# Kernel optimization log

Measured on AMD Instinct MI355X. Metric: run time of the kernel, lower is better.

The kernel has to match this reference:

```python
import jax, jax.numpy as jnp
import numpy as np

B, N, DIM = 4, 2048, 64  # batch, seq_len (== gate out dim), model dim (== dim_head)
H, DH = 8, 64            # heads, dim_head


def setup_inputs() -> dict:
    key = jax.random.key(0)
    ks = jax.random.split(key, 12)
    inner = H * DH
    inp = {
        'q': jax.random.normal(ks[0], (B, N, DIM), jnp.float32),
        'k': jax.random.normal(ks[1], (B, N, DIM), jnp.float32),
        'v': jax.random.normal(ks[2], (B, N, DIM), jnp.float32),
        'Wq': jax.random.normal(ks[3], (inner, DIM), jnp.float32) * 0.05,
        'Wk': jax.random.normal(ks[4], (inner, DIM), jnp.float32) * 0.05,
        'Wv': jax.random.normal(ks[5], (inner, DIM), jnp.float32) * 0.05,
        'Wo': jax.random.normal(ks[6], (DIM, inner), jnp.float32) * 0.05,
        'bo': jax.random.normal(ks[7], (DIM,), jnp.float32) * 0.05,
        'Wg': jax.random.normal(ks[8], (N, DIM), jnp.float32) * 0.05,
        's_local': jnp.float32(1.0),
        's_long': jnp.float32(1.0),
        # recurrent compressive-memory state; positive to avoid 0/0 of zero-init buffers
        'mem': jax.random.uniform(ks[9], (H, DH, DH), jnp.float32) + 0.5,
        'mem_norm': jax.random.uniform(ks[10], (H, N, 1), jnp.float32) + 0.5,
    }
    return inp


def _heads(x, W):
    # x: (B,N,DIM) @ W.T (DIM, H*DH) -> (B,H,N,DH)
    y = x @ W.T
    return y.reshape(x.shape[0], x.shape[1], H, DH).transpose(0, 2, 1, 3)


def reference(q, k, v, Wq, Wk, Wv, Wo, bo, Wg, s_local, s_long, mem, mem_norm):
    scale = DH ** -0.5
    qh, kh, vh = _heads(q, Wq), _heads(k, Wk), _heads(v, Wv)  # (B,H,N,DH)

    # local softmax attention, down-gated by (1 - sigmoid(local scalar))
    sim = jnp.einsum('bhnd,bhmd->bhnm', qh, kh) * scale
    local_attn = jax.nn.softmax(sim, axis=-1) * (1.0 - jax.nn.sigmoid(s_local))

    # query compressive memory: elu(q) @ M / (elu(q) * norm)
    eq = jax.nn.elu(qh)
    mem_q = jnp.einsum('bhnd,hde->bhne', eq, mem) / (eq * mem_norm[None])  # (B,H,N,DH)
    gated = jax.nn.sigmoid(s_long) * jnp.einsum('bhnd,md->bhnm', mem_q, Wg)  # (B,H,N,N)

    attn = local_attn + gated
    out = jnp.einsum('bhnm,bhmd->bhnd', attn, vh)
    out = out.transpose(0, 2, 1, 3).reshape(q.shape[0], q.shape[1], H * DH)
    out = out @ Wo.T + bo  # (B,N,DIM)

    # memory update (state side effect in the original forward)
    ek = jax.nn.elu(kh)
    v_term = vh - jnp.einsum('bhnd,hde->bhne', ek, mem) / (ek * mem_norm[None])
    new_mem = mem[None] + jnp.einsum('bhnd,bhne->bhde', ek, v_term)  # (B,H,DH,DH)
    new_norm = ek.sum(-1)  # (B,H,N)
    return out, new_mem, new_norm
```

## Files before the change

kernel.cpp:

```cpp
#include <hip/hip_runtime.h>
#include <math.h>


#define B_   4
#define N_   2048
#define H_   8
#define BH_  32
#define KP   72
#define KPV  68
#define SCLK 0.18033688f

typedef __bf16 bf16x8 __attribute__((ext_vector_type(8)));
typedef __bf16 bf16x4 __attribute__((ext_vector_type(4)));
typedef short  s16x4  __attribute__((ext_vector_type(4)));
typedef float  f32x4  __attribute__((ext_vector_type(4)));

__device__ __forceinline__ float eluf(float x) {
    return x > 0.0f ? x : expm1f(x);
}

__device__ __forceinline__ float fexp2(float x) {
    return __builtin_amdgcn_exp2f(x);
}

__device__ __forceinline__ f32x4 mfma16(bf16x4 a, bf16x4 b, f32x4 c) {
#if __has_builtin(__builtin_amdgcn_mfma_f32_16x16x16_bf16)
    return __builtin_amdgcn_mfma_f32_16x16x16_bf16(a, b, c, 0, 0, 0);
#else
    s16x4 ai, bi;
    __builtin_memcpy(&ai, &a, 8);
    __builtin_memcpy(&bi, &b, 8);
    return __builtin_amdgcn_mfma_f32_16x16x16bf16_1k(ai, bi, c, 0, 0, 0);
#endif
}

__global__ __launch_bounds__(256) void k_proj(
    const float* __restrict__ q, const float* __restrict__ k, const float* __restrict__ v,
    const float* __restrict__ Wq, const float* __restrict__ Wk, const float* __restrict__ Wv,
    __bf16* __restrict__ qb, float* __restrict__ kh, __bf16* __restrict__ kb,
    __bf16* __restrict__ vb, __bf16* __restrict__ vbT)
{
    const int which = blockIdx.z;
    const int h    = blockIdx.y;
    const int row0 = blockIdx.x * 64;
    const int tid  = threadIdx.x;
    const int b = row0 >> 11, nb = row0 & 2047;

    __shared__ __align__(16) float  AsT[64][68];
    __shared__ __align__(16) float  WsT[64][68];
    __shared__ __align__(16) __bf16 Cs[64 * 72];

    if (which == 2) {
        const int w = tid >> 6, lane = tid & 63;
        const int quad = lane >> 4, m = lane & 15;
        const float* ar = v + (size_t)(row0 + w * 16 + m) * 64;
        bf16x8 a0, a1;
        #pragma unroll
        for (int j = 0; j < 8; ++j) {
            a0[j] = (__bf16)ar[quad * 8 + j];
            a1[j] = (__bf16)ar[32 + quad * 8 + j];
        }
        f32x4 acc[4];
        #pragma unroll
        for (int t = 0; t < 4; ++t) {
            const float* wr = Wv + (size_t)(h * 64 + t * 16 + m) * 64;
            bf16x8 b0, b1;
            #pragma unroll
            for (int j = 0; j < 8; ++j) {
                b0[j] = (__bf16)wr[quad * 8 + j];
                b1[j] = (__bf16)wr[32 + quad * 8 + j];
            }
            f32x4 z = {0.f, 0.f, 0.f, 0.f};
            z = __builtin_amdgcn_mfma_f32_16x16x32_bf16(a0, b0, z, 0, 0, 0);
            acc[t] = __builtin_amdgcn_mfma_f32_16x16x32_bf16(a1, b1, z, 0, 0, 0);
        }
        #pragma unroll
        for (int t = 0; t < 4; ++t)
            #pragma unroll
            for (int r = 0; r < 4; ++r)
                Cs[(w * 16 + quad * 4 + r) * 72 + t * 16 + m] = (__bf16)acc[t][r];
        __syncthreads();
        const int rr = tid >> 2, csg = (tid & 3) * 16;
        bf16x8 r0 = *(const bf16x8*)&Cs[rr * 72 + csg];
        bf16x8 r1 = *(const bf16x8*)&Cs[rr * 72 + csg + 8];
        size_t gb = ((((size_t)b * H_ + h) * N_ + nb + rr) << 6) + csg;
        *(bf16x8*)&vb[gb]     = r0;
        *(bf16x8*)&vb[gb + 8] = r1;
        const int e = tid >> 2, ns = (tid & 3) * 16;
        bf16x8 t0, t1;
        #pragma unroll
        for (int j = 0; j < 8; ++j) {
            t0[j] = Cs[(ns + j) * 72 + e];
            t1[j] = Cs[(ns + 8 + j) * 72 + e];
        }
        size_t base = (((size_t)b * H_ + h) * 64 + e) * (size_t)N_ + nb + ns;
        *(bf16x8*)&vbT[base]     = t0;
        *(bf16x8*)&vbT[base + 8] = t1;
        return;
    }

    const float* __restrict__ src = (which == 0) ? q : k;
    const float* __restrict__ W   = (which == 0) ? Wq : Wk;
    for (int s = 0; s < 16; ++s) {
        int flat = s * 256 + tid;
        int r = flat >> 6, d = flat & 63;
        AsT[d][r] = src[(size_t)(row0 + r) * 64 + d];
        WsT[d][r] = W[(size_t)(h * 64 + r) * 64 + d];
    }
    __syncthreads();

    const int ty = tid >> 4, tx = tid & 15;
    float acc[4][4];
    #pragma unroll
    for (int i = 0; i < 4; ++i)
        #pragma unroll
        for (int j = 0; j < 4; ++j) acc[i][j] = 0.0f;
    for (int kd = 0; kd < 64; ++kd) {
        float4 a4 = *(const float4*)&AsT[kd][ty * 4];
        float4 w4 = *(const float4*)&WsT[kd][tx * 4];
        float a[4] = {a4.x, a4.y, a4.z, a4.w};
        float w[4] = {w4.x, w4.y, w4.z, w4.w};
        #pragma unroll
        for (int i = 0; i < 4; ++i)
            #pragma unroll
            for (int j = 0; j < 4; ++j) acc[i][j] = fmaf(a[i], w[j], acc[i][j]);
    }

    if (which == 0) {
        #pragma unroll
        for (int i = 0; i < 4; ++i) {
            size_t idx = ((((size_t)b * H_ + h) * N_ + nb + ty * 4 + i) << 6) + tx * 4;
            bf16x4 o4 = {(__bf16)acc[i][0], (__bf16)acc[i][1],
                         (__bf16)acc[i][2], (__bf16)acc[i][3]};
            *(bf16x4*)&qb[idx] = o4;
        }
    } else {
        #pragma unroll
        for (int i = 0; i < 4; ++i) {
            size_t idx = ((((size_t)b * H_ + h) * N_ + nb + ty * 4 + i) << 6) + tx * 4;
            *(float4*)&kh[idx] = make_float4(acc[i][0], acc[i][1], acc[i][2], acc[i][3]);
            bf16x4 o4 = {(__bf16)(acc[i][0] * SCLK), (__bf16)(acc[i][1] * SCLK),
                         (__bf16)(acc[i][2] * SCLK), (__bf16)(acc[i][3] * SCLK)};
            *(bf16x4*)&kb[idx] = o4;
        }
    }
}

__global__ __launch_bounds__(256) void k_memacc(
    const float* __restrict__ kh, const __bf16* __restrict__ vb,
    const float* __restrict__ mem, const float* __restrict__ mem_norm,
    float* __restrict__ pmem, float* __restrict__ out_norm)
{
    const int chunk = blockIdx.x;
    const int bh    = blockIdx.y;
    const int h     = bh & 7;
    const int n0    = chunk * 128;

    __shared__ __align__(16) __bf16 memT_hi[64 * KP], memT_lo[64 * KP];
    __shared__ __align__(16) __bf16 ekn_hi[64 * KP],  ekn_lo[64 * KP];
    __shared__ __align__(16) __bf16 ekT_hi[64 * KP],  ekT_lo[64 * KP];
    __shared__ __align__(16) __bf16 vtT_hi[64 * KP],  vtT_lo[64 * KP];

    const int tid  = threadIdx.x;
    const int w    = tid >> 6, lane = tid & 63;
    const int quad = lane >> 4, m = lane & 15;

    for (int s = 0; s < 16; ++s) {
        int flat = s * 256 + tid;
        int d = flat >> 6, e = flat & 63;
        float mv = mem[(size_t)h * 4096 + flat];
        __bf16 hi = (__bf16)mv;
        memT_hi[e * KP + d] = hi;
        memT_lo[e * KP + d] = (__bf16)(mv - (float)hi);
    }

    bf16x8 onesv;
    #pragma unroll
    for (int j = 0; j < 8; ++j) onesv[j] = (m == 0) ? (__bf16)1.0f : (__bf16)0.0f;

    f32x4 accM[4];
    #pragma unroll
    for (int t = 0; t < 4; ++t) { f32x4 z = {0.f, 0.f, 0.f, 0.f}; accM[t] = z; }
    __syncthreads();

    for (int sub = 0; sub < 2; ++sub) {
        const int nb = n0 + sub * 64;
        for (int rr = w; rr < 64; rr += 4) {
            const int n = nb + rr;
            float ekv = eluf(kh[((size_t)bh * N_ + n) * 64 + lane]);
            __bf16 hi = (__bf16)ekv;
            __bf16 lo = (__bf16)(ekv - (float)hi);
            ekn_hi[rr * KP + lane] = hi;
            ekn_lo[rr * KP + lane] = lo;
            ekT_hi[lane * KP + rr] = hi;
            ekT_lo[lane * KP + rr] = lo;
        }
        __syncthreads();

        f32x4 km[4];
        #pragma unroll
        for (int t = 0; t < 4; ++t) { f32x4 z = {0.f, 0.f, 0.f, 0.f}; km[t] = z; }
        f32x4 nsum = {0.f, 0.f, 0.f, 0.f};
        #pragma unroll
        for (int c2 = 0; c2 < 2; ++c2) {
            bf16x8 Ah = *(const bf16x8*)&ekn_hi[(w * 16 + m) * KP + c2 * 32 + quad * 8];
            bf16x8 Al = *(const bf16x8*)&ekn_lo[(w * 16 + m) * KP + c2 * 32 + quad * 8];
            nsum = __builtin_amdgcn_mfma_f32_16x16x32_bf16(Ah, onesv, nsum, 0, 0, 0);
            nsum = __builtin_amdgcn_mfma_f32_16x16x32_bf16(Al, onesv, nsum, 0, 0, 0);
            #pragma unroll
            for (int et = 0; et < 4; ++et) {
                bf16x8 Bh = *(const bf16x8*)&memT_hi[(et * 16 + m) * KP + c2 * 32 + quad * 8];
                bf16x8 Bl = *(const bf16x8*)&memT_lo[(et * 16 + m) * KP + c2 * 32 + quad * 8];
                km[et] = __builtin_amdgcn_mfma_f32_16x16x32_bf16(Al, Bh, km[et], 0, 0, 0);
                km[et] = __builtin_amdgcn_mfma_f32_16x16x32_bf16(Ah, Bl, km[et], 0, 0, 0);
                km[et] = __builtin_amdgcn_mfma_f32_16x16x32_bf16(Ah, Bh, km[et], 0, 0, 0);
            }
        }
        if (m == 0) {
            #pragma unroll
            for (int r = 0; r < 4; ++r)
                out_norm[(size_t)bh * N_ + nb + w * 16 + quad * 4 + r] = nsum[r];
        }
        float nrmv[4];
        #pragma unroll
        for (int r = 0; r < 4; ++r)
            nrmv[r] = mem_norm[(size_t)h * N_ + nb + w * 16 + quad * 4 + r];
        #pragma unroll
        for (int et = 0; et < 4; ++et) {
            #pragma unroll
            for (int r = 0; r < 4; ++r) {
                const int nl = w * 16 + quad * 4 + r;
                const int e  = et * 16 + m;
                float vh  = (float)vb[((size_t)bh * N_ + nb + nl) * 64 + e];
                float ekv = (float)ekn_hi[nl * KP + e] + (float)ekn_lo[nl * KP + e];
                float vt  = vh - km[et][r] * __builtin_amdgcn_rcpf(ekv * nrmv[r]);
                __bf16 hi = (__bf16)vt;
                vtT_hi[e * KP + nl] = hi;
                vtT_lo[e * KP + nl] = (__bf16)(vt - (float)hi);
            }
        }
        __syncthreads();

        #pragma unroll
        for (int c2 = 0; c2 < 2; ++c2) {
            bf16x8 Ah = *(const bf16x8*)&ekT_hi[(w * 16 + m) * KP + c2 * 32 + quad * 8];
            bf16x8 Al = *(const bf16x8*)&ekT_lo[(w * 16 + m) * KP + c2 * 32 + quad * 8];
            #pragma unroll
            for (int et = 0; et < 4; ++et) {
                bf16x8 Bh = *(const bf16x8*)&vtT_hi[(et * 16 + m) * KP + c2 * 32 + quad * 8];
                bf16x8 Bl = *(const bf16x8*)&vtT_lo[(et * 16 + m) * KP + c2 * 32 + quad * 8];
                accM[et] = __builtin_amdgcn_mfma_f32_16x16x32_bf16(Al, Bh, accM[et], 0, 0, 0);
                accM[et] = __builtin_amdgcn_mfma_f32_16x16x32_bf16(Ah, Bl, accM[et], 0, 0, 0);
                accM[et] = __builtin_amdgcn_mfma_f32_16x16x32_bf16(Ah, Bh, accM[et], 0, 0, 0);
            }
        }
        __syncthreads();
    }

    const size_t base = ((size_t)chunk * BH_ + bh) * 4096;
    #pragma unroll
    for (int et = 0; et < 4; ++et)
        #pragma unroll
        for (int r = 0; r < 4; ++r)
            pmem[base + (size_t)(w * 16 + quad * 4 + r) * 64 + et * 16 + m] =
                accM[et][r];
}

__global__ __launch_bounds__(256) void k_gv(
    const float* __restrict__ Wg, const __bf16* __restrict__ vbT,
    float* __restrict__ pGv)
{
    const int chunk = blockIdx.x;
    const int bh    = blockIdx.y;
    const int n0    = chunk * 128;
    __shared__ __align__(16) __bf16 WgT[64 * 136];
    const int tid  = threadIdx.x;
    const int w    = tid >> 6, lane = tid & 63;
    const int quad = lane >> 4, m = tid & 15;

    for (int s = 0; s < 8; ++s) {
        int f4 = s * 256 + tid;
        int n = f4 >> 4, dg = (f4 & 15) * 4;
        float4 wv = *(const float4*)&Wg[(size_t)(n0 + n) * 64 + dg];
        WgT[(dg + 0) * 136 + n] = (__bf16)wv.x;
        WgT[(dg + 1) * 136 + n] = (__bf16)wv.y;
        WgT[(dg + 2) * 136 + n] = (__bf16)wv.z;
        WgT[(dg + 3) * 136 + n] = (__bf16)wv.w;
    }
    __syncthreads();

    f32x4 acc[4];
    #pragma unroll
    for (int t = 0; t < 4; ++t) { f32x4 z = {0.f, 0.f, 0.f, 0.f}; acc[t] = z; }
    #pragma unroll
    for (int c = 0; c < 4; ++c) {
        bf16x8 Af = *(const bf16x8*)&WgT[(w * 16 + m) * 136 + c * 32 + quad * 8];
        #pragma unroll
        for (int et = 0; et < 4; ++et) {
            bf16x8 Bf = *(const bf16x8*)&vbT[((size_t)bh * 64 + et * 16 + m) * N_ +
                                             n0 + c * 32 + quad * 8];
            acc[et] = __builtin_amdgcn_mfma_f32_16x16x32_bf16(Af, Bf, acc[et], 0, 0, 0);
        }
    }
    const size_t base = ((size_t)chunk * BH_ + bh) * 4096;
    #pragma unroll
    for (int et = 0; et < 4; ++et)
        #pragma unroll
        for (int r = 0; r < 4; ++r)
            pGv[base + (size_t)(w * 16 + quad * 4 + r) * 64 + et * 16 + m] =
                acc[et][r];
}

__global__ __launch_bounds__(256) void k_reduce(
    const float* __restrict__ mem, const float* __restrict__ pmem,
    const float* __restrict__ pGv, float* __restrict__ out_mem, float* __restrict__ Gv)
{
    const int idx = blockIdx.x * 256 + threadIdx.x;
    const int bh = idx >> 12, h = bh & 7, de = idx & 4095;
    float sm = mem[(size_t)h * 4096 + de];
    float sg = 0.0f;
    #pragma unroll
    for (int c = 0; c < 16; ++c) {
        sm += pmem[(size_t)c * 131072 + idx];
        sg += pGv[(size_t)c * 131072 + idx];
    }
    out_mem[idx] = sm;
    Gv[idx] = sg;
}

__global__ __launch_bounds__(512, 2) void k_flash(
    const __bf16* __restrict__ qb, const __bf16* __restrict__ kb,
    const __bf16* __restrict__ vbT, const float* __restrict__ mem,
    const float* __restrict__ mem_norm, const float* __restrict__ Gv,
    const float* __restrict__ s_local_p, const float* __restrict__ s_long_p,
    __bf16* __restrict__ o)
{
    const int n0 = blockIdx.x * 256;
    const int bh = blockIdx.y;
    const int h  = bh & 7;
    const __bf16* __restrict__ kbp = kb  + (size_t)bh * N_ * 64;
    const __bf16* __restrict__ vtp = vbT + (size_t)bh * 64 * N_;

    __shared__ __align__(16) char smem[56832];
    __bf16* const KbA = (__bf16*)(smem);
    __bf16* const KbB = (__bf16*)(smem + 9216);
    __bf16* const VTA = (__bf16*)(smem + 18432);
    __bf16* const VTB = (__bf16*)(smem + 27136);
    __bf16* const MT  = (__bf16*)(smem);
    __bf16* const GT  = (__bf16*)(smem + 9216);
    __bf16* const Pw  = (__bf16*)(smem + 17920);
    float*  const lsl   = (float*)(smem + 54784);
    float*  const nrm_l = (float*)(smem + 55808);

    const int tid  = threadIdx.x;
    const int w    = tid >> 6, lane = tid & 63;
    const int quad = lane >> 4, m = lane & 15;
    const float gl   = 1.0f - 1.0f / (1.0f + __expf(-s_local_p[0]));
    const float sigg = 1.0f / (1.0f + __expf(-s_long_p[0]));

    if (tid < 256) nrm_l[tid] = mem_norm[(size_t)h * N_ + n0 + tid];

    const size_t q0 = ((size_t)bh * N_ + n0 + w * 32 + m) * 64;
    const size_t q1 = q0 + 16 * 64;
    bf16x8 qa00 = *(const bf16x8*)&qb[q0 + quad * 8];
    bf16x8 qa01 = *(const bf16x8*)&qb[q0 + 32 + quad * 8];
    bf16x8 qa10 = *(const bf16x8*)&qb[q1 + quad * 8];
    bf16x8 qa11 = *(const bf16x8*)&qb[q1 + 32 + quad * 8];

    f32x4 O0[4], O1[4];
    #pragma unroll
    for (int t = 0; t < 4; ++t) {
        f32x4 z = {0.f, 0.f, 0.f, 0.f};
        O0[t] = z; O1[t] = z;
    }
    f32x4 nacc0 = {0.f, 0.f, 0.f, 0.f}, nacc1 = {0.f, 0.f, 0.f, 0.f};
    bf16x4 ones4;
    #pragma unroll
    for (int j = 0; j < 4; ++j) ones4[j] = (m == 0) ? (__bf16)1.0f : (__bf16)0.0f;
    const int pr0 = w * 32, pr1 = w * 32 + 16;

    const int srow = tid >> 3, scg = (tid & 7) * 8;
    bf16x8 pk0 = *(const bf16x8*)&kbp[(size_t)srow * 64 + scg];
    bf16x8 pv0 = *(const bf16x8*)&vtp[(size_t)srow * N_ + scg];
    *(bf16x8*)&KbA[srow * KP + scg]  = pk0;
    *(bf16x8*)&VTA[srow * KPV + scg] = pv0;
    {
        const size_t kn = (size_t)(64 + srow) * 64 + scg;
        const size_t vn = (size_t)srow * N_ + 64 + scg;
        pk0 = *(const bf16x8*)&kbp[kn];
        pv0 = *(const bf16x8*)&vtp[vn];
    }

    for (int c = 0; c < 32; ++c) {
        asm volatile("s_waitcnt lgkmcnt(0)" ::: "memory");
        __builtin_amdgcn_s_barrier();
        if (c + 1 < 32) {
            __bf16* Kn = (c & 1) ? KbA : KbB;
            __bf16* Vn = (c & 1) ? VTA : VTB;
            *(bf16x8*)&Kn[srow * KP + scg]  = pk0;
            *(bf16x8*)&Vn[srow * KPV + scg] = pv0;
        }
        if (c + 2 < 32) {
            const size_t kn = (size_t)((c + 2) * 64 + srow) * 64 + scg;
            const size_t vn = (size_t)srow * N_ + (c + 2) * 64 + scg;
            pk0 = *(const bf16x8*)&kbp[kn];
            pv0 = *(const bf16x8*)&vtp[vn];
        }
        const __bf16* Kc = (c & 1) ? KbB : KbA;
        const __bf16* Vc = (c & 1) ? VTB : VTA;

        f32x4 s0[4], s1[4];
        __builtin_amdgcn_s_setprio(1);
        #pragma unroll
        for (int t = 0; t < 4; ++t) {
            bf16x8 ka0 = *(const bf16x8*)&Kc[(t * 16 + m) * KP + quad * 8];
            bf16x8 ka1 = *(const bf16x8*)&Kc[(t * 16 + m) * KP + 32 + quad * 8];
            f32x4 z = {0.f, 0.f, 0.f, 0.f};
            z = __builtin_amdgcn_mfma_f32_16x16x32_bf16(ka0, qa00, z, 0, 0, 0);
            s0[t] = __builtin_amdgcn_mfma_f32_16x16x32_bf16(ka1, qa01, z, 0, 0, 0);
            f32x4 z2 = {0.f, 0.f, 0.f, 0.f};
            z2 = __builtin_amdgcn_mfma_f32_16x16x32_bf16(ka0, qa10, z2, 0, 0, 0);
            s1[t] = __builtin_amdgcn_mfma_f32_16x16x32_bf16(ka1, qa11, z2, 0, 0, 0);
        }
        __builtin_amdgcn_s_setprio(0);

        bf16x4 pa0[4], pa1[4];
        #pragma unroll
        for (int t = 0; t < 4; ++t) {
            float p0 = fexp2(s0[t][0]), p1 = fexp2(s0[t][1]);
            float p2 = fexp2(s0[t][2]), p3 = fexp2(s0[t][3]);
            bf16x4 pk = {(__bf16)p0, (__bf16)p1, (__bf16)p2, (__bf16)p3};
            pa0[t] = pk;
            float r0 = fexp2(s1[t][0]), r1 = fexp2(s1[t][1]);
            float r2 = fexp2(s1[t][2]), r3 = fexp2(s1[t][3]);
            bf16x4 rk = {(__bf16)r0, (__bf16)r1, (__bf16)r2, (__bf16)r3};
            pa1[t] = rk;
        }

        __builtin_amdgcn_s_setprio(1);
        #pragma unroll
        for (int t = 0; t < 4; ++t) {
            nacc0 = mfma16(pa0[t], ones4, nacc0);
            nacc1 = mfma16(pa1[t], ones4, nacc1);
            #pragma unroll
            for (int et = 0; et < 4; ++et) {
                bf16x4 vb4 = *(const bf16x4*)&Vc[(et * 16 + m) * KPV + t * 16 + quad * 4];
                O0[et] = mfma16(pa0[t], vb4, O0[et]);
                O1[et] = mfma16(pa1[t], vb4, O1[et]);
            }
        }
        __builtin_amdgcn_s_setprio(0);
    }

    if (m == 0) {
        #pragma unroll
        for (int r = 0; r < 4; ++r) {
            lsl[pr0 + quad * 4 + r] = nacc0[r];
            lsl[pr1 + quad * 4 + r] = nacc1[r];
        }
    }

    __syncthreads();
    {
        const float* mp = mem + (size_t)h * 4096;
        const float* gp = Gv + (size_t)bh * 4096;
        #pragma unroll
        for (int s2 = 0; s2 < 2; ++s2) {
            int idx = s2 * 512 + tid;
            int e = idx & 63, d4 = (idx >> 6) << 2;
            bf16x4 mv, gv;
            #pragma unroll
            for (int j = 0; j < 4; ++j) {
                mv[j] = (__bf16)mp[(size_t)(d4 + j) * 64 + e];
                gv[j] = (__bf16)gp[(size_t)(d4 + j) * 64 + e];
            }
            *(bf16x4*)&MT[e * KP + d4] = mv;
            *(bf16x4*)&GT[e * KPV + d4] = gv;
        }
    }
    __syncthreads();

    __bf16* op = o + ((size_t)bh * N_ + n0) * 64;
    #pragma unroll
    for (int s = 0; s < 2; ++s) {
        const int prs = w * 32 + s * 16;
        bf16x8 ea0, ea1;
        #pragma unroll
        for (int j = 0; j < 8; ++j) {
            ea0[j] = (__bf16)eluf((float)(s == 0 ? qa00[j] : qa10[j]));
            ea1[j] = (__bf16)eluf((float)(s == 0 ? qa01[j] : qa11[j]));
        }
        f32x4 num[4];
        #pragma unroll
        for (int t = 0; t < 4; ++t) {
            bf16x8 b0 = *(const bf16x8*)&MT[(t * 16 + m) * KP + quad * 8];
            bf16x8 b1 = *(const bf16x8*)&MT[(t * 16 + m) * KP + 32 + quad * 8];
            f32x4 z = {0.f, 0.f, 0.f, 0.f};
            z = __builtin_amdgcn_mfma_f32_16x16x32_bf16(ea0, b0, z, 0, 0, 0);
            num[t] = __builtin_amdgcn_mfma_f32_16x16x32_bf16(ea1, b1, z, 0, 0, 0);
        }
        *(bf16x8*)&Pw[(prs + m) * KP + quad * 8]      = ea0;
        *(bf16x8*)&Pw[(prs + m) * KP + 32 + quad * 8] = ea1;
        asm volatile("s_waitcnt lgkmcnt(0)" ::: "memory");
        float mq[4][4];
        #pragma unroll
        for (int t = 0; t < 4; ++t)
            #pragma unroll
            for (int r = 0; r < 4; ++r) {
                float eqv = (float)Pw[(prs + quad * 4 + r) * KP + t * 16 + m];
                mq[t][r] = num[t][r] / (eqv * nrm_l[prs + quad * 4 + r]);
            }
        #pragma unroll
        for (int t = 0; t < 4; ++t)
            #pragma unroll
            for (int r = 0; r < 4; ++r)
                Pw[(prs + quad * 4 + r) * KP + t * 16 + m] = (__bf16)mq[t][r];
        asm volatile("s_waitcnt lgkmcnt(0)" ::: "memory");
        bf16x8 ma0 = *(const bf16x8*)&Pw[(prs + m) * KP + quad * 8];
        bf16x8 ma1 = *(const bf16x8*)&Pw[(prs + m) * KP + 32 + quad * 8];

        #pragma unroll
        for (int t = 0; t < 4; ++t) {
            bf16x8 g0 = *(const bf16x8*)&GT[(t * 16 + m) * KPV + quad * 8];
            bf16x8 g1 = *(const bf16x8*)&GT[(t * 16 + m) * KPV + 32 + quad * 8];
            f32x4 z = {0.f, 0.f, 0.f, 0.f};
            z = __builtin_amdgcn_mfma_f32_16x16x32_bf16(ma0, g0, z, 0, 0, 0);
            f32x4 o2 = __builtin_amdgcn_mfma_f32_16x16x32_bf16(ma1, g1, z, 0, 0, 0);
            #pragma unroll
            for (int r = 0; r < 4; ++r) {
                const int qr = prs + quad * 4 + r;
                float val = ((s == 0) ? O0[t][r] : O1[t][r]) * (gl / lsl[qr])
                            + sigg * o2[r];
                op[(size_t)qr * 64 + t * 16 + m] = (__bf16)val;
            }
        }
    }
}

__global__ __launch_bounds__(256) void k_outproj(
    const __bf16* __restrict__ o, const float* __restrict__ Wo,
    const float* __restrict__ bo, float* __restrict__ out)
{
    const int row0 = blockIdx.x * 64;
    const int b = row0 >> 11, nb = row0 & 2047;
    __shared__ __align__(16) __bf16 WoS[64 * 296];
    const int tid  = threadIdx.x;
    const int w    = tid >> 6, lane = tid & 63;
    const int quad = lane >> 4, m = lane & 15;

    f32x4 acc[4];
    #pragma unroll
    for (int t = 0; t < 4; ++t) { f32x4 z = {0.f, 0.f, 0.f, 0.f}; acc[t] = z; }

    for (int half = 0; half < 2; ++half) {
        for (int s2 = 0; s2 < 16; ++s2) {
            int f4 = s2 * 256 + tid;
            int n = f4 >> 6, k4 = (f4 & 63) * 4;
            float4 wv = *(const float4*)&Wo[(size_t)n * 512 + half * 256 + k4];
            bf16x4 o4 = {(__bf16)wv.x, (__bf16)wv.y, (__bf16)wv.z, (__bf16)wv.w};
            *(bf16x4*)&WoS[n * 296 + k4] = o4;
        }
        __syncthreads();
        for (int kbk = 0; kbk < 8; ++kbk) {
            const int kbk2 = half * 8 + kbk;
            const int hc = kbk2 >> 1;
            size_t arow = (((size_t)b * H_ + hc) * N_ + nb + w * 16 + m);
            bf16x8 af = *(const bf16x8*)&o[arow * 64 + (kbk2 & 1) * 32 + quad * 8];
            #pragma unroll
            for (int t = 0; t < 4; ++t) {
                bf16x8 bf_ = *(const bf16x8*)&WoS[(t * 16 + m) * 296 + kbk * 32 + quad * 8];
                acc[t] = __builtin_amdgcn_mfma_f32_16x16x32_bf16(af, bf_, acc[t], 0, 0, 0);
            }
        }
        __syncthreads();
    }
    #pragma unroll
    for (int t = 0; t < 4; ++t) {
        float bias = bo[t * 16 + m];
        #pragma unroll
        for (int r = 0; r < 4; ++r)
            out[(size_t)(row0 + w * 16 + quad * 4 + r) * 64 + t * 16 + m] =
                acc[t][r] + bias;
    }
}

extern "C" void kernel_launch(void* const* d_in, const int* in_sizes, int n_in,
                              void* d_out, int out_size, void* d_ws, size_t ws_size,
                              hipStream_t stream)
{
    const float* q        = (const float*)d_in[0];
    const float* k        = (const float*)d_in[1];
    const float* v        = (const float*)d_in[2];
    const float* Wq       = (const float*)d_in[3];
    const float* Wk       = (const float*)d_in[4];
    const float* Wv       = (const float*)d_in[5];
    const float* Wo       = (const float*)d_in[6];
    const float* bo       = (const float*)d_in[7];
    const float* Wg       = (const float*)d_in[8];
    const float* s_local  = (const float*)d_in[9];
    const float* s_long   = (const float*)d_in[10];
    const float* mem      = (const float*)d_in[11];
    const float* mem_norm = (const float*)d_in[12];

    float* ws = (float*)d_ws;
    float*  kh  = ws;
    __bf16* qb  = (__bf16*)(ws + 4194304);
    __bf16* kb  = (__bf16*)(ws + 6291456);
    __bf16* vb  = (__bf16*)(ws + 8388608);
    __bf16* vbT = (__bf16*)(ws + 10485760);
    float*  Gv  = ws + 12582912;
    float*  pm  = ws + 12713984;
    float*  pg  = ws + 14811136;
    __bf16* o   = (__bf16*)(ws + 12713984);

    float* out      = (float*)d_out;
    float* out_mem  = out + 524288;
    float* out_norm = out + 655360;

    k_proj   <<<dim3(128, 8, 3), 256, 0, stream>>>(q, k, v, Wq, Wk, Wv,
                                                   qb, kh, kb, vb, vbT);
    k_memacc <<<dim3(16, 32),    256, 0, stream>>>(kh, vb, mem, mem_norm,
                                                   pm, out_norm);
    k_gv     <<<dim3(16, 32),    256, 0, stream>>>(Wg, vbT, pg);
    k_reduce <<<dim3(512),       256, 0, stream>>>(mem, pm, pg, out_mem, Gv);
    k_flash  <<<dim3(8, 32),     512, 0, stream>>>(qb, kb, vbT, mem, mem_norm, Gv,
                                                   s_local, s_long, o);
    k_outproj<<<dim3(128),       256, 0, stream>>>(o, Wo, bo, out);
}
```

Measured before the change: 202.6 us.

## Split projection kernel, enlarge QK register tiles, replace MFMA row-sum with VALU sums

The fused q/k/v projection kernel is split into a QK kernel and a V kernel. The QK kernel now computes 128x128 tiles with an 8x8 per-thread register block and float4 global loads, staging K in two halves of 32. In the flash kernel, the softmax denominator moves from extra MFMA ops against a ones vector to scalar adds followed by cross-lane shuffles, and the s_setprio hints plus the manual waitcnt/barrier are replaced with __syncthreads. These changes aim to cut MFMA work and raise reuse in the projection, at the cost of more registers, an extra launch, and more VALU work.

```diff
diff --git a/kernel.cpp b/kernel.cpp
--- a/kernel.cpp
+++ b/kernel.cpp
@@ -34,116 +34,139 @@
 #endif
 }
 
-__global__ __launch_bounds__(256) void k_proj(
-    const float* __restrict__ q, const float* __restrict__ k, const float* __restrict__ v,
-    const float* __restrict__ Wq, const float* __restrict__ Wk, const float* __restrict__ Wv,
-    __bf16* __restrict__ qb, float* __restrict__ kh, __bf16* __restrict__ kb,
+__global__ __launch_bounds__(256) void k_projqk(
+    const float* __restrict__ q, const float* __restrict__ k,
+    const float* __restrict__ Wq, const float* __restrict__ Wk,
+    __bf16* __restrict__ qb, float* __restrict__ kh, __bf16* __restrict__ kb)
+{
+    const int which = blockIdx.z;
+    const int hp   = blockIdx.y;
+    const int row0 = blockIdx.x * 128;
+    const int tid  = threadIdx.x;
+    const int b = row0 >> 11, nb = row0 & 2047;
+
+    __shared__ __align__(16) float AsT[32][132];
+    __shared__ __align__(16) float WsT[32][132];
+
+    const float* __restrict__ src = (which == 0) ? q : k;
+    const float* __restrict__ W   = (which == 0) ? Wq : Wk;
+
+    const int ty = tid >> 4, tx = tid & 15;
+    float acc[8][8];
+    #pragma unroll
+    for (int i = 0; i < 8; ++i)
+        #pragma unroll
+        for (int j = 0; j < 8; ++j) acc[i][j] = 0.0f;
+
+    for (int half = 0; half < 2; ++half) {
+        __syncthreads();
+        for (int s = 0; s < 4; ++s) {
+            int f = s * 256 + tid;
+            int r = f >> 3, d4 = (f & 7) * 4;
+            float4 av = *(const float4*)&src[(size_t)(row0 + r) * 64 + half * 32 + d4];
+            AsT[d4 + 0][r] = av.x; AsT[d4 + 1][r] = av.y;
+            AsT[d4 + 2][r] = av.z; AsT[d4 + 3][r] = av.w;
+            float4 wv = *(const float4*)&W[(size_t)(hp * 128 + r) * 64 + half * 32 + d4];
+            WsT[d4 + 0][r] = wv.x; WsT[d4 + 1][r] = wv.y;
+            WsT[d4 + 2][r] = wv.z; WsT[d4 + 3][r] = wv.w;
+        }
+        __syncthreads();
+        for (int kd = 0; kd < 32; ++kd) {
+            float4 a0 = *(const float4*)&AsT[kd][ty * 8];
+            float4 a1 = *(const float4*)&AsT[kd][ty * 8 + 4];
+            float4 w0 = *(const float4*)&WsT[kd][tx * 8];
+            float4 w1 = *(const float4*)&WsT[kd][tx * 8 + 4];
+            float a[8]  = {a0.x, a0.y, a0.z, a0.w, a1.x, a1.y, a1.z, a1.w};
+            float wv[8] = {w0.x, w0.y, w0.z, w0.w, w1.x, w1.y, w1.z, w1.w};
+            #pragma unroll
+            for (int i = 0; i < 8; ++i)
+                #pragma unroll
+                for (int j = 0; j < 8; ++j)
+                    acc[i][j] = fmaf(a[i], wv[j], acc[i][j]);
+        }
+    }
+
+    const int h   = hp * 2 + (tx >> 3);
+    const int dh0 = (tx & 7) * 8;
+    if (which == 0) {
+        #pragma unroll
+        for (int i = 0; i < 8; ++i) {
+            size_t idx = ((((size_t)b * H_ + h) * N_ + nb + ty * 8 + i) << 6) + dh0;
+            bf16x8 o8;
+            #pragma unroll
+            for (int j = 0; j < 8; ++j) o8[j] = (__bf16)acc[i][j];
+            *(bf16x8*)&qb[idx] = o8;
+        }
+    } else {
+        #pragma unroll
+        for (int i = 0; i < 8; ++i) {
+            size_t idx = ((((size_t)b * H_ + h) * N_ + nb + ty * 8 + i) << 6) + dh0;
+            *(float4*)&kh[idx]     = make_float4(acc[i][0], acc[i][1], acc[i][2], acc[i][3]);
+            *(float4*)&kh[idx + 4] = make_float4(acc[i][4], acc[i][5], acc[i][6], acc[i][7]);
+            bf16x8 o8;
+            #pragma unroll
+            for (int j = 0; j < 8; ++j) o8[j] = (__bf16)(acc[i][j] * SCLK);
+            *(bf16x8*)&kb[idx] = o8;
+        }
+    }
+}
+
+__global__ __launch_bounds__(256) void k_projv(
+    const float* __restrict__ v, const float* __restrict__ Wv,
     __bf16* __restrict__ vb, __bf16* __restrict__ vbT)
 {
-    const int which = blockIdx.z;
     const int h    = blockIdx.y;
     const int row0 = blockIdx.x * 64;
     const int tid  = threadIdx.x;
     const int b = row0 >> 11, nb = row0 & 2047;
 
-    __shared__ __align__(16) float  AsT[64][68];
-    __shared__ __align__(16) float  WsT[64][68];
     __shared__ __align__(16) __bf16 Cs[64 * 72];
 
-    if (which == 2) {
-        const int w = tid >> 6, lane = tid & 63;
-        const int quad = lane >> 4, m = lane & 15;
-        const float* ar = v + (size_t)(row0 + w * 16 + m) * 64;
-        bf16x8 a0, a1;
+    const int w = tid >> 6, lane = tid & 63;
+    const int quad = lane >> 4, m = lane & 15;
+    const float* ar = v + (size_t)(row0 + w * 16 + m) * 64;
+    bf16x8 a0, a1;
+    #pragma unroll
+    for (int j = 0; j < 8; ++j) {
+        a0[j] = (__bf16)ar[quad * 8 + j];
+        a1[j] = (__bf16)ar[32 + quad * 8 + j];
+    }
+    f32x4 acc[4];
+    #pragma unroll
+    for (int t = 0; t < 4; ++t) {
+        const float* wr = Wv + (size_t)(h * 64 + t * 16 + m) * 64;
+        bf16x8 b0, b1;
         #pragma unroll
         for (int j = 0; j < 8; ++j) {
-            a0[j] = (__bf16)ar[quad * 8 + j];
-            a1[j] = (__bf16)ar[32 + quad * 8 + j];
-        }
-        f32x4 acc[4];
-        #pragma unroll
-        for (int t = 0; t < 4; ++t) {
-            const float* wr = Wv + (size_t)(h * 64 + t * 16 + m) * 64;
-            bf16x8 b0, b1;
-            #pragma unroll
-            for (int j = 0; j < 8; ++j) {
-                b0[j] = (__bf16)wr[quad * 8 + j];
-                b1[j] = (__bf16)wr[32 + quad * 8 + j];
-            }
-            f32x4 z = {0.f, 0.f, 0.f, 0.f};
-            z = __builtin_amdgcn_mfma_f32_16x16x32_bf16(a0, b0, z, 0, 0, 0);
-            acc[t] = __builtin_amdgcn_mfma_f32_16x16x32_bf16(a1, b1, z, 0, 0, 0);
-        }
-        #pragma unroll
-        for (int t = 0; t < 4; ++t)
-            #pragma unroll
-            for (int r = 0; r < 4; ++r)
-                Cs[(w * 16 + quad * 4 + r) * 72 + t * 16 + m] = (__bf16)acc[t][r];
-        __syncthreads();
-        const int rr = tid >> 2, csg = (tid & 3) * 16;
-        bf16x8 r0 = *(const bf16x8*)&Cs[rr * 72 + csg];
-        bf16x8 r1 = *(const bf16x8*)&Cs[rr * 72 + csg + 8];
-        size_t gb = ((((size_t)b * H_ + h) * N_ + nb + rr) << 6) + csg;
-        *(bf16x8*)&vb[gb]     = r0;
-        *(bf16x8*)&vb[gb + 8] = r1;
-        const int e = tid >> 2, ns = (tid & 3) * 16;
-        bf16x8 t0, t1;
-        #pragma unroll
-        for (int j = 0; j < 8; ++j) {
-            t0[j] = Cs[(ns + j) * 72 + e];
-            t1[j] = Cs[(ns + 8 + j) * 72 + e];
-        }
-        size_t base = (((size_t)b * H_ + h) * 64 + e) * (size_t)N_ + nb + ns;
-        *(bf16x8*)&vbT[base]     = t0;
-        *(bf16x8*)&vbT[base + 8] = t1;
-        return;
-    }
-
-    const float* __restrict__ src = (which == 0) ? q : k;
-    const float* __restrict__ W   = (which == 0) ? Wq : Wk;
-    for (int s = 0; s < 16; ++s) {
-        int flat = s * 256 + tid;
-        int r = flat >> 6, d = flat & 63;
-        AsT[d][r] = src[(size_t)(row0 + r) * 64 + d];
-        WsT[d][r] = W[(size_t)(h * 64 + r) * 64 + d];
-    }
+            b0[j] = (__bf16)wr[quad * 8 + j];
+            b1[j] = (__bf16)wr[32 + quad * 8 + j];
+        }
+        f32x4 z = {0.f, 0.f, 0.f, 0.f};
+        z = __builtin_amdgcn_mfma_f32_16x16x32_bf16(a0, b0, z, 0, 0, 0);
+        acc[t] = __builtin_amdgcn_mfma_f32_16x16x32_bf16(a1, b1, z, 0, 0, 0);
+    }
+    #pragma unroll
+    for (int t = 0; t < 4; ++t)
+        #pragma unroll
+        for (int r = 0; r < 4; ++r)
+            Cs[(w * 16 + quad * 4 + r) * 72 + t * 16 + m] = (__bf16)acc[t][r];
     __syncthreads();
-
-    const int ty = tid >> 4, tx = tid & 15;
-    float acc[4][4];
-    #pragma unroll
-    for (int i = 0; i < 4; ++i)
-        #pragma unroll
-        for (int j = 0; j < 4; ++j) acc[i][j] = 0.0f;
-    for (int kd = 0; kd < 64; ++kd) {
-        float4 a4 = *(const float4*)&AsT[kd][ty * 4];
-        float4 w4 = *(const float4*)&WsT[kd][tx * 4];
-        float a[4] = {a4.x, a4.y, a4.z, a4.w};
-        float w[4] = {w4.x, w4.y, w4.z, w4.w};
-        #pragma unroll
-        for (int i = 0; i < 4; ++i)
-            #pragma unroll
-            for (int j = 0; j < 4; ++j) acc[i][j] = fmaf(a[i], w[j], acc[i][j]);
-    }
-
-    if (which == 0) {
-        #pragma unroll
-        for (int i = 0; i < 4; ++i) {
-            size_t idx = ((((size_t)b * H_ + h) * N_ + nb + ty * 4 + i) << 6) + tx * 4;
-            bf16x4 o4 = {(__bf16)acc[i][0], (__bf16)acc[i][1],
-                         (__bf16)acc[i][2], (__bf16)acc[i][3]};
-            *(bf16x4*)&qb[idx] = o4;
-        }
-    } else {
-        #pragma unroll
-        for (int i = 0; i < 4; ++i) {
-            size_t idx = ((((size_t)b * H_ + h) * N_ + nb + ty * 4 + i) << 6) + tx * 4;
-            *(float4*)&kh[idx] = make_float4(acc[i][0], acc[i][1], acc[i][2], acc[i][3]);
-            bf16x4 o4 = {(__bf16)(acc[i][0] * SCLK), (__bf16)(acc[i][1] * SCLK),
-                         (__bf16)(acc[i][2] * SCLK), (__bf16)(acc[i][3] * SCLK)};
-            *(bf16x4*)&kb[idx] = o4;
-        }
-    }
+    const int rr = tid >> 2, csg = (tid & 3) * 16;
+    bf16x8 r0 = *(const bf16x8*)&Cs[rr * 72 + csg];
+    bf16x8 r1 = *(const bf16x8*)&Cs[rr * 72 + csg + 8];
+    size_t gb = ((((size_t)b * H_ + h) * N_ + nb + rr) << 6) + csg;
+    *(bf16x8*)&vb[gb]     = r0;
+    *(bf16x8*)&vb[gb + 8] = r1;
+    const int e = tid >> 2, ns = (tid & 3) * 16;
+    bf16x8 t0, t1;
+    #pragma unroll
+    for (int j = 0; j < 8; ++j) {
+        t0[j] = Cs[(ns + j) * 72 + e];
+        t1[j] = Cs[(ns + 8 + j) * 72 + e];
+    }
+    size_t base = (((size_t)b * H_ + h) * 64 + e) * (size_t)N_ + nb + ns;
+    *(bf16x8*)&vbT[base]     = t0;
+    *(bf16x8*)&vbT[base + 8] = t1;
 }
 
 __global__ __launch_bounds__(256) void k_memacc(
@@ -373,10 +396,7 @@
         f32x4 z = {0.f, 0.f, 0.f, 0.f};
         O0[t] = z; O1[t] = z;
     }
-    f32x4 nacc0 = {0.f, 0.f, 0.f, 0.f}, nacc1 = {0.f, 0.f, 0.f, 0.f};
-    bf16x4 ones4;
-    #pragma unroll
-    for (int j = 0; j < 4; ++j) ones4[j] = (m == 0) ? (__bf16)1.0f : (__bf16)0.0f;
+    float lsum0 = 0.f, lsum1 = 0.f;
     const int pr0 = w * 32, pr1 = w * 32 + 16;
 
     const int srow = tid >> 3, scg = (tid & 7) * 8;
@@ -392,8 +412,7 @@
     }
 
     for (int c = 0; c < 32; ++c) {
-        asm volatile("s_waitcnt lgkmcnt(0)" ::: "memory");
-        __builtin_amdgcn_s_barrier();
+        __syncthreads();
         if (c + 1 < 32) {
             __bf16* Kn = (c & 1) ? KbA : KbB;
             __bf16* Vn = (c & 1) ? VTA : VTB;
@@ -410,7 +429,6 @@
         const __bf16* Vc = (c & 1) ? VTB : VTA;
 
         f32x4 s0[4], s1[4];
-        __builtin_amdgcn_s_setprio(1);
         #pragma unroll
         for (int t = 0; t < 4; ++t) {
             bf16x8 ka0 = *(const bf16x8*)&Kc[(t * 16 + m) * KP + quad * 8];
@@ -422,26 +440,24 @@
             z2 = __builtin_amdgcn_mfma_f32_16x16x32_bf16(ka0, qa10, z2, 0, 0, 0);
             s1[t] = __builtin_amdgcn_mfma_f32_16x16x32_bf16(ka1, qa11, z2, 0, 0, 0);
         }
-        __builtin_amdgcn_s_setprio(0);
 
         bf16x4 pa0[4], pa1[4];
         #pragma unroll
         for (int t = 0; t < 4; ++t) {
             float p0 = fexp2(s0[t][0]), p1 = fexp2(s0[t][1]);
             float p2 = fexp2(s0[t][2]), p3 = fexp2(s0[t][3]);
+            lsum0 += p0 + p1 + p2 + p3;
             bf16x4 pk = {(__bf16)p0, (__bf16)p1, (__bf16)p2, (__bf16)p3};
             pa0[t] = pk;
             float r0 = fexp2(s1[t][0]), r1 = fexp2(s1[t][1]);
             float r2 = fexp2(s1[t][2]), r3 = fexp2(s1[t][3]);
+            lsum1 += r0 + r1 + r2 + r3;
             bf16x4 rk = {(__bf16)r0, (__bf16)r1, (__bf16)r2, (__bf16)r3};
             pa1[t] = rk;
         }
 
-        __builtin_amdgcn_s_setprio(1);
         #pragma unroll
         for (int t = 0; t < 4; ++t) {
-            nacc0 = mfma16(pa0[t], ones4, nacc0);
-            nacc1 = mfma16(pa1[t], ones4, nacc1);
             #pragma unroll
             for (int et = 0; et < 4; ++et) {
                 bf16x4 vb4 = *(const bf16x4*)&Vc[(et * 16 + m) * KPV + t * 16 + quad * 4];
@@ -449,16 +465,11 @@
                 O1[et] = mfma16(pa1[t], vb4, O1[et]);
             }
         }
-        __builtin_amdgcn_s_setprio(0);
-    }
-
-    if (m == 0) {
-        #pragma unroll
-        for (int r = 0; r < 4; ++r) {
-            lsl[pr0 + quad * 4 + r] = nacc0[r];
-            lsl[pr1 + quad * 4 + r] = nacc1[r];
-        }
-    }
+    }
+
+    lsum0 += __shfl_xor(lsum0, 16, 64); lsum0 += __shfl_xor(lsum0, 32, 64);
+    lsum1 += __shfl_xor(lsum1, 16, 64); lsum1 += __shfl_xor(lsum1, 32, 64);
+    if (lane < 16) { lsl[pr0 + lane] = lsum0; lsl[pr1 + lane] = lsum1; }
 
     __syncthreads();
     {
@@ -617,13 +628,13 @@
     float* out_mem  = out + 524288;
     float* out_norm = out + 655360;
 
-    k_proj   <<<dim3(128, 8, 3), 256, 0, stream>>>(q, k, v, Wq, Wk, Wv,
-                                                   qb, kh, kb, vb, vbT);
-    k_memacc <<<dim3(16, 32),    256, 0, stream>>>(kh, vb, mem, mem_norm,
-                                                   pm, out_norm);
-    k_gv     <<<dim3(16, 32),    256, 0, stream>>>(Wg, vbT, pg);
-    k_reduce <<<dim3(512),       256, 0, stream>>>(mem, pm, pg, out_mem, Gv);
-    k_flash  <<<dim3(8, 32),     512, 0, stream>>>(qb, kb, vbT, mem, mem_norm, Gv,
-                                                   s_local, s_long, o);
-    k_outproj<<<dim3(128),       256, 0, stream>>>(o, Wo, bo, out);
-}
+    k_projqk <<<dim3(64, 4, 2), 256, 0, stream>>>(q, k, Wq, Wk, qb, kh, kb);
+    k_projv  <<<dim3(128, 8),   256, 0, stream>>>(v, Wv, vb, vbT);
+    k_memacc <<<dim3(16, 32),   256, 0, stream>>>(kh, vb, mem, mem_norm,
+                                                  pm, out_norm);
+    k_gv     <<<dim3(16, 32),   256, 0, stream>>>(Wg, vbT, pg);
+    k_reduce <<<dim3(512),      256, 0, stream>>>(mem, pm, pg, out_mem, Gv);
+    k_flash  <<<dim3(8, 32),    512, 0, stream>>>(qb, kb, vbT, mem, mem_norm, Gv,
+                                                  s_local, s_long, o);
+    k_outproj<<<dim3(128),      256, 0, stream>>>(o, Wo, bo, out);
+}
```

Result: slower. 207.3 us (+2.3%).
